# Performance work log

Measured on AMD Instinct MI355X. Metric: run time of the kernel, lower is better.

The kernel has to match this reference:

```python
import jax, jax.numpy as jnp
import numpy as np

EPS = 1e-15
MAX_NORM = 1.0 - 1e-5

def _norm(x):
    return jnp.sqrt(jnp.maximum(jnp.sum(x * x, -1, keepdims=True), EPS))

def project(x):
    n = _norm(x)
    return jnp.where(n > MAX_NORM, x * (MAX_NORM / n), x)

def mobius_add(x, y):
    x2 = jnp.sum(x * x, -1, keepdims=True)
    y2 = jnp.sum(y * y, -1, keepdims=True)
    xy = jnp.sum(x * y, -1, keepdims=True)
    num = (1.0 + 2.0 * xy + y2) * x + (1.0 - x2) * y
    den = 1.0 + 2.0 * xy + x2 * y2
    return num / jnp.maximum(den, EPS)

def expmap0(u):
    n = _norm(u)
    return jnp.tanh(n) * u / n

def expmap(u, p):
    lam = 2.0 / jnp.maximum(1.0 - jnp.sum(p * p, -1, keepdims=True), EPS)
    n = _norm(u)
    return mobius_add(p, jnp.tanh(0.5 * lam * n) * u / n)

def logmap(x, p):
    sub = mobius_add(-p, x)
    n = _norm(sub)
    lam = 2.0 / jnp.maximum(1.0 - jnp.sum(p * p, -1, keepdims=True), EPS)
    return (2.0 / lam) * jnp.arctanh(jnp.minimum(n, MAX_NORM)) * sub / n

def seg_mean(msg, idx, n):
    s = jax.ops.segment_sum(msg, idx, num_segments=n)
    c = jax.ops.segment_sum(jnp.ones((idx.shape[0], 1), msg.dtype), idx, num_segments=n)
    return s / jnp.maximum(c, 1.0)  # zero in-degree -> 0, matching DGL mean


def setup_inputs() -> dict:
    N_ENT, N_USR, N_ITM, N_REL, D = 100000, 50000, 30000, 40, 64
    E_KG, E_CF = 800000, 600000
    key = jax.random.key(0)
    ks = jax.random.split(key, 12)
    return {
        "entity_embed": 0.1 * jax.random.normal(ks[0], (N_ENT, D), jnp.float32),
        "user_embed": 0.1 * jax.random.normal(ks[1], (N_USR, D), jnp.float32),
        "relation_emb": 0.1 * jax.random.normal(ks[2], (N_REL, D), jnp.float32),
        "W1": jax.random.normal(ks[3], (D, D), jnp.float32) / np.sqrt(D),
        "W2": jax.random.normal(ks[4], (D, D), jnp.float32) / np.sqrt(D),
        "kg_src": jax.random.randint(ks[5], (E_KG,), 0, N_ENT, jnp.int32),
        "kg_dst": jax.random.randint(ks[6], (E_KG,), 0, N_ENT, jnp.int32),
        "kg_type": jax.random.randint(ks[7], (E_KG,), 0, N_REL - 2, jnp.int32),
        "iu_src": jax.random.randint(ks[8], (E_CF,), 0, N_ITM, jnp.int32),
        "iu_dst": N_ITM + jax.random.randint(ks[9], (E_CF,), 0, N_USR, jnp.int32),
        "ui_src": N_ITM + jax.random.randint(ks[10], (E_CF,), 0, N_USR, jnp.int32),
        "ui_dst": jax.random.randint(ks[11], (E_CF,), 0, N_ITM, jnp.int32),
        "n_items": N_ITM,
    }


def reference(entity_embed, user_embed, relation_emb, W1, W2,
              kg_src, kg_dst, kg_type, iu_src, iu_dst, ui_src, ui_dst, n_items):
    n_ent = entity_embed.shape[0]
    n_usr = user_embed.shape[0]
    N = n_items + n_usr

    # --- per-edge hyperbolic UDF (tan_sum) on the KG graph ---
    p = expmap0(entity_embed[kg_src])                 # [E, d] tangent origin at src
    dst_h = expmap(entity_embed[kg_dst], p)
    rel_h = expmap(relation_emb[kg_type + 2], p)
    tan_sum = logmap(project(mobius_add(dst_h, rel_h)), p)
    # sg_inv reverses edges, so mean groups by the ORIGINAL src node
    out = seg_mean(tan_sum, kg_src, n_ent)            # [n_ent, d]

    # --- CF scatter-means over item/user bipartite graphs ---
    cat_nodes = jnp.concatenate([out[:n_items], user_embed], axis=0)  # [N, d]
    u = seg_mean(cat_nodes[iu_src], iu_dst, N)[n_items:]              # [n_usr, d]

    norm_all = jnp.sum(cat_nodes * cat_nodes, -1, keepdims=True)      # ||.||^2, [N,1]
    node_n = cat_nodes / (norm_all + 1e-6)
    msg = node_n[ui_src] * norm_all[ui_dst]                           # u_mul_v
    i_cf = seg_mean(msg, ui_dst, N)[:n_items]                         # [n_items, d]

    # --- gated fusion ---
    out_items = out[:n_items]
    gi = jax.nn.sigmoid(out_items @ W1.T + i_cf @ W2.T)
    item_emb_fusion = gi * out_items + (1.0 - gi) * i_cf

    return (jnp.concatenate([item_emb_fusion, out[n_items:]], axis=0), u, out_items)
```

## Files before the change

### kernel.cpp

```cpp
#include <hip/hip_runtime.h>
#include <cstdint>

#define EPSF 1e-15f
#define MAXN (1.0f - 1e-5f)
#define BSH 9

typedef __attribute__((ext_vector_type(8))) short bf16x8;
typedef __attribute__((ext_vector_type(4))) float f32x4;
typedef unsigned short ushort_t;

__device__ __forceinline__ float wsum64(float v) {
    v += __shfl_xor(v, 1);
    v += __shfl_xor(v, 2);
    v += __shfl_xor(v, 4);
    v += __shfl_xor(v, 8);
    v += __shfl_xor(v, 16);
    v += __shfl_xor(v, 32);
    return v;
}

__device__ __forceinline__ float dot4(float4 a, float4 b) {
    return a.x * b.x + a.y * b.y + a.z * b.z + a.w * b.w;
}

__device__ __forceinline__ float frcp(float x) {
    return __builtin_amdgcn_rcpf(x);
}

__device__ __forceinline__ float tanh_f(float x) {
    x = fminf(x, 10.f);
    float t = __expf(2.f * x);
    return (t - 1.f) * frcp(t + 1.f);
}

__device__ __forceinline__ float atanh_f(float x) {
    return 0.5f * __logf((1.f + x) * frcp(1.f - x));
}

__device__ __forceinline__ ushort_t f2bf(float f) {
    uint32_t b = __float_as_uint(f);
    b = (b + 0x7FFF + ((b >> 16) & 1)) >> 16;
    return (ushort_t)b;
}

__device__ __forceinline__ float bf2f(ushort_t h) {
    return __uint_as_float((uint32_t)h << 16);
}

__device__ __forceinline__ bf16x8 pack8(const float* __restrict__ p) {
    float4 lo = *(const float4*)p;
    float4 hi = *(const float4*)(p + 4);
    bf16x8 r;
    r[0] = (short)f2bf(lo.x); r[1] = (short)f2bf(lo.y);
    r[2] = (short)f2bf(lo.z); r[3] = (short)f2bf(lo.w);
    r[4] = (short)f2bf(hi.x); r[5] = (short)f2bf(hi.y);
    r[6] = (short)f2bf(hi.z); r[7] = (short)f2bf(hi.w);
    return r;
}

__global__ __launch_bounds__(256) void cvt3_k(
        const float* __restrict__ ent, const float* __restrict__ usr,
        const float* __restrict__ rel,
        ushort_t* __restrict__ entH, ushort_t* __restrict__ usrH,
        ushort_t* __restrict__ relH, long nE, long nU, long nR) {
    long i = ((long)blockIdx.x * blockDim.x + threadIdx.x) * 8;
    const float* s; ushort_t* d; long off;
    if (i < nE) { s = ent; d = entH; off = i; }
    else if (i < nE + nU) { s = usr; d = usrH; off = i - nE; }
    else if (i < nE + nU + nR) { s = rel; d = relH; off = i - nE - nU; }
    else return;
    float4 a = *(const float4*)(s + off);
    float4 b = *(const float4*)(s + off + 4);
    ushort4 lo; lo.x = f2bf(a.x); lo.y = f2bf(a.y); lo.z = f2bf(a.z); lo.w = f2bf(a.w);
    ushort4 hi; hi.x = f2bf(b.x); hi.y = f2bf(b.y); hi.z = f2bf(b.z); hi.w = f2bf(b.w);
    *(ushort4*)(d + off) = lo;
    *(ushort4*)(d + off + 4) = hi;
}


__global__ __launch_bounds__(256) void p1_hist_k(
        const int* __restrict__ kg_src, const int* __restrict__ iu_dst,
        const int* __restrict__ ui_dst, int* __restrict__ H,
        int E_kg, int E_iu, int E_ui, int n_items, int S1, int SU, int nbins) {
    __shared__ int h[512];
    int tid = threadIdx.x;
    h[tid] = 0; h[tid + 256] = 0;
    __syncthreads();
    long tot = (long)E_kg + E_iu + E_ui;
    long b0 = (long)blockIdx.x * 2048 + tid;
#pragma unroll
    for (int j = 0; j < 8; ++j) {
        long t = b0 + (long)j * 256;
        if (t < tot) {
            int slot;
            if (t < E_kg) slot = kg_src[t];
            else if (t < (long)E_kg + E_iu) slot = S1 + iu_dst[t - E_kg] - n_items;
            else slot = S1 + SU + ui_dst[t - E_kg - E_iu];
            atomicAdd(&h[slot >> BSH], 1);
        }
    }
    __syncthreads();
    int* row = H + (size_t)blockIdx.x * nbins;
    if (tid < nbins) row[tid] = h[tid];
    if (tid + 256 < nbins) row[tid + 256] = h[tid + 256];
}

__global__ __launch_bounds__(256) void p2a_scan_k(int* __restrict__ H,
        int* __restrict__ binTotal, int NBLK, int nbins) {
    int bin = blockIdx.x, tid = threadIdx.x;
    int lane = tid & 63, w = tid >> 6;
    __shared__ int wtot[4];
    int carry = 0;
    for (int c0 = 0; c0 < NBLK; c0 += 256) {
        int idx = c0 + tid;
        int v = (idx < NBLK) ? H[(size_t)idx * nbins + bin] : 0;
        int inc = v;
#pragma unroll
        for (int off = 1; off < 64; off <<= 1) {
            int u = __shfl_up(inc, off);
            if (lane >= off) inc += u;
        }
        if (lane == 63) wtot[w] = inc;
        __syncthreads();
        int woff = 0;
        for (int i = 0; i < w; ++i) woff += wtot[i];
        int ctot = wtot[0] + wtot[1] + wtot[2] + wtot[3];
        if (idx < NBLK) H[(size_t)idx * nbins + bin] = carry + woff + inc - v;
        carry += ctot;
        __syncthreads();
    }
    if (tid == 0) binTotal[bin] = carry;
}

__global__ __launch_bounds__(512) void p2b_bins_k(const int* __restrict__ binTotal,
        int* __restrict__ binStart, int nbins) {
    int tid = threadIdx.x, lane = tid & 63, w = tid >> 6;
    __shared__ int wtot[8];
    int v = (tid < nbins) ? binTotal[tid] : 0;
    int inc = v;
#pragma unroll
    for (int off = 1; off < 64; off <<= 1) {
        int u = __shfl_up(inc, off);
        if (lane >= off) inc += u;
    }
    if (lane == 63) wtot[w] = inc;
    __syncthreads();
    int woff = 0;
    for (int i = 0; i < w; ++i) woff += wtot[i];
    if (tid < nbins) binStart[tid] = woff + inc - v;
    if (tid == 0) {
        int tot = 0;
        for (int i = 0; i < 8; ++i) tot += wtot[i];
        binStart[nbins] = tot;
    }
}

__global__ __launch_bounds__(256) void p3_scat_k(
        const int* __restrict__ kg_src, const int* __restrict__ kg_dst,
        const int* __restrict__ kg_typ, const int* __restrict__ iu_src,
        const int* __restrict__ iu_dst, const int* __restrict__ ui_src,
        const int* __restrict__ ui_dst,
        const int* __restrict__ H, const int* __restrict__ binStart,
        int2* __restrict__ recA,
        int E_kg, int E_iu, int E_ui, int n_items, int S1, int SU, int nbins) {
    __shared__ int off[512];
    int tid = threadIdx.x;
    const int* row = H + (size_t)blockIdx.x * nbins;
    if (tid < nbins) off[tid] = binStart[tid] + row[tid];
    if (tid + 256 < nbins) off[tid + 256] = binStart[tid + 256] + row[tid + 256];
    __syncthreads();
    long tot = (long)E_kg + E_iu + E_ui;
    long b0 = (long)blockIdx.x * 2048 + tid;
#pragma unroll
    for (int j = 0; j < 8; ++j) {
        long t = b0 + (long)j * 256;
        if (t < tot) {
            int slot, aux;
            if (t < E_kg) {
                slot = kg_src[t];
                aux = kg_dst[t] | ((kg_typ[t] + 2) << 18);
            } else if (t < (long)E_kg + E_iu) {
                long e = t - E_kg;
                slot = S1 + iu_dst[e] - n_items;
                aux = iu_src[e];
            } else {
                long e = t - E_kg - E_iu;
                slot = S1 + SU + ui_dst[e];
                aux = ui_src[e];
            }
            int pos = atomicAdd(&off[slot >> BSH], 1);
            recA[pos] = make_int2(slot, aux);
        }
    }
}

__global__ __launch_bounds__(256) void p4_sort_k(
        const int2* __restrict__ recA, const int* __restrict__ binStart,
        int2* __restrict__ recB, int* __restrict__ deg, int* __restrict__ base,
        int nbins) {
    int b = blockIdx.x, tid = threadIdx.x;
    int lane = tid & 63, w = tid >> 6;
    int lo = binStart[b], cnt = binStart[b + 1] - lo;
    __shared__ int h[512];
    __shared__ int pre[512];
    __shared__ int wtot[4];
    h[tid] = 0; h[tid + 256] = 0;
    __syncthreads();
    for (int i = tid; i < cnt; i += 256)
        atomicAdd(&h[recA[lo + i].x & 511], 1);
    __syncthreads();
    int v1 = h[tid];
    int inc = v1;
#pragma unroll
    for (int off = 1; off < 64; off <<= 1) {
        int u = __shfl_up(inc, off);
        if (lane >= off) inc += u;
    }
    if (lane == 63) wtot[w] = inc;
    __syncthreads();
    int woff = 0;
    for (int i = 0; i < w; ++i) woff += wtot[i];
    int T1 = wtot[0] + wtot[1] + wtot[2] + wtot[3];
    int p1 = woff + inc - v1;
    __syncthreads();
    int v2 = h[tid + 256];
    inc = v2;
#pragma unroll
    for (int off = 1; off < 64; off <<= 1) {
        int u = __shfl_up(inc, off);
        if (lane >= off) inc += u;
    }
    if (lane == 63) wtot[w] = inc;
    __syncthreads();
    woff = 0;
    for (int i = 0; i < w; ++i) woff += wtot[i];
    int p2 = T1 + woff + inc - v2;
    pre[tid] = p1; pre[tid + 256] = p2;
    int slot0 = (b << BSH) + tid;
    deg[slot0] = v1;       base[slot0] = lo + p1;
    deg[slot0 + 256] = v2; base[slot0 + 256] = lo + p2;
    __syncthreads();
    for (int i = tid; i < cnt; i += 256) {
        int2 r = recA[lo + i];
        int p = atomicAdd(&pre[r.x & 511], 1);
        recB[lo + p] = r;
    }
}


__global__ __launch_bounds__(256) void kg_edge_fused_k(const float* __restrict__ ent,
                          const float* __restrict__ rel,
                          const int2* __restrict__ rec,
                          float4* __restrict__ payload,
                          int nE) {
    int w = blockIdx.x * 4 + (threadIdx.x >> 6);
    int l = threadIdx.x & 63;
    int slot = w * 16 + (l >> 2);
    if (slot >= nE) return;
    int j0 = l & 3;
    int2 rc = rec[slot];
    int s = rc.x, d = rc.y & 0x3FFFF, ty = rc.y >> 18;
    const float4* pu = (const float4*)(ent + (size_t)s * 64);
    const float4* pv = (const float4*)(ent + (size_t)d * 64);
    const float4* pr = (const float4*)(rel + (size_t)ty * 64);

    float uu = 0.f, vv = 0.f, rr = 0.f, uv = 0.f, ur = 0.f, vr = 0.f;
#pragma unroll
    for (int i = 0; i < 4; ++i) {
        float4 a = pu[4 * i + j0], b = pv[4 * i + j0], c = pr[4 * i + j0];
        uu += dot4(a, a); vv += dot4(b, b); rr += dot4(c, c);
        uv += dot4(a, b); ur += dot4(a, c); vr += dot4(b, c);
    }
#pragma unroll
    for (int m = 1; m < 4; m <<= 1) {
        uu += __shfl_xor(uu, m);
        vv += __shfl_xor(vv, m);
        rr += __shfl_xor(rr, m);
        uv += __shfl_xor(uv, m);
        ur += __shfl_xor(ur, m);
        vr += __shfl_xor(vr, m);
    }

    float n0 = sqrtf(fmaxf(uu, EPSF));
    float cp = tanh_f(n0) * frcp(n0);
    float p2 = cp * cp * uu;
    float om_p2 = 1.f - p2;
    float lam = 2.f * frcp(fmaxf(om_p2, EPSF));

    float nv = sqrtf(fmaxf(vv, EPSF));
    float cd = tanh_f(0.5f * lam * nv) * frcp(nv);
    float wd2 = cd * cd * vv;
    float pwd = cp * cd * uv;
    float iDd = frcp(fmaxf(1.f + 2.f * pwd + p2 * wd2, EPSF));
    float a1 = (1.f + 2.f * pwd + wd2) * cp * iDd;
    float b1 = om_p2 * cd * iDd;

    float nr = sqrtf(fmaxf(rr, EPSF));
    float cr = tanh_f(0.5f * lam * nr) * frcp(nr);
    float wr2 = cr * cr * rr;
    float pwr = cp * cr * ur;
    float iDr = frcp(fmaxf(1.f + 2.f * pwr + p2 * wr2, EPSF));
    float a2 = (1.f + 2.f * pwr + wr2) * cp * iDr;
    float c2 = om_p2 * cr * iDr;

    float x2 = a1 * a1 * uu + 2.f * a1 * b1 * uv + b1 * b1 * vv;
    float y2 = a2 * a2 * uu + 2.f * a2 * c2 * ur + c2 * c2 * rr;
    float xy = a1 * a2 * uu + a1 * c2 * ur + b1 * a2 * uv + b1 * c2 * vr;
    float iden = frcp(fmaxf(1.f + 2.f * xy + x2 * y2, EPSF));
    float E = (1.f + 2.f * xy + y2) * iden;
    float F = (1.f - x2) * iden;
    float zu = E * a1 + F * a2;
    float zv = E * b1;
    float zr = F * c2;

    float z2 = zu * zu * uu + zv * zv * vv + zr * zr * rr
             + 2.f * (zu * zv * uv + zu * zr * ur + zv * zr * vr);
    float nz = sqrtf(fmaxf(z2, EPSF));
    if (nz > MAXN) {
        float sc = MAXN * frcp(nz);
        zu *= sc; zv *= sc; zr *= sc;
        z2 *= sc * sc;
    }

    float mxy = -cp * (zu * uu + zv * uv + zr * ur);
    float idenl = frcp(fmaxf(1.f + 2.f * mxy + p2 * z2, EPSF));
    float G = (1.f + 2.f * mxy + z2) * idenl;
    float H = om_p2 * idenl;
    float su = -G * cp + H * zu;
    float sv = H * zv;
    float sr = H * zr;

    float ns2 = su * su * uu + sv * sv * vv + sr * sr * rr
              + 2.f * (su * sv * uv + su * sr * ur + sv * sr * vr);
    float ns = sqrtf(fmaxf(ns2, EPSF));
    float k = fmaxf(om_p2, EPSF) * atanh_f(fminf(ns, MAXN)) * frcp(ns);

    if (j0 == 0) {
        payload[slot] = make_float4(k * sv, k * sr, k * su, __int_as_float(rc.y));
    }
}

__global__ void kg_gather_k(const float* __restrict__ ent,
                            const ushort_t* __restrict__ entH,
                            const ushort_t* __restrict__ relH,
                            const int* __restrict__ deg,
                            const int* __restrict__ base,
                            const float4* __restrict__ payload,
                            float* __restrict__ out_final,
                            float* __restrict__ out_items,
                            ushort_t* __restrict__ catH,
                            float* __restrict__ normv,
                            int n_items, int n) {
    int w = blockIdx.x * (blockDim.x >> 6) + (threadIdx.x >> 6);
    int i0 = w * 2;
    if (i0 >= n) return;
    bool has1 = (i0 + 1 < n);
    int l = threadIdx.x & 63;
    int b0 = base[i0];
    int d0 = deg[i0];
    int d1 = has1 ? deg[i0 + 1] : 0;
    int cnt = d0 + d1;
    int split = b0 + d0;
    float acc0 = 0.f, as0 = 0.f, acc1 = 0.f, as1 = 0.f;
    int q = 0;
    for (; q + 8 <= cnt; q += 8) {
        float4 p[8]; float vv[8], rr_[8];
#pragma unroll
        for (int j = 0; j < 8; ++j) p[j] = payload[b0 + q + j];
#pragma unroll
        for (int j = 0; j < 8; ++j) {
            int wd = __float_as_int(p[j].w);
            vv[j] = bf2f(entH[(size_t)(wd & 0x3FFFF) * 64 + l]);
            rr_[j] = bf2f(relH[(size_t)(wd >> 18) * 64 + l]);
        }
#pragma unroll
        for (int j = 0; j < 8; ++j) {
            float t = p[j].x * vv[j] + p[j].y * rr_[j];
            bool s0 = (b0 + q + j) < split;
            acc0 += s0 ? t : 0.f;
            acc1 += s0 ? 0.f : t;
            as0 += s0 ? p[j].z : 0.f;
            as1 += s0 ? 0.f : p[j].z;
        }
    }
    for (; q < cnt; ++q) {
        float4 p = payload[b0 + q];
        int wd = __float_as_int(p.w);
        float t = p.x * bf2f(entH[(size_t)(wd & 0x3FFFF) * 64 + l])
                + p.y * bf2f(relH[(size_t)(wd >> 18) * 64 + l]);
        bool s0 = (b0 + q) < split;
        acc0 += s0 ? t : 0.f;
        acc1 += s0 ? 0.f : t;
        as0 += s0 ? p.z : 0.f;
        as1 += s0 ? 0.f : p.z;
    }
    {
        float v = (acc0 + as0 * ent[(size_t)i0 * 64 + l]) * frcp(fmaxf((float)d0, 1.f));
        if (i0 < n_items) {
            out_items[(size_t)i0 * 64 + l] = v;
            catH[(size_t)i0 * 64 + l] = f2bf(v);
            float s2 = wsum64(v * v);
            if (l == 0) normv[i0] = s2;
        } else {
            out_final[(size_t)i0 * 64 + l] = v;
        }
    }
    if (has1) {
        int i1 = i0 + 1;
        float v = (acc1 + as1 * ent[(size_t)i1 * 64 + l]) * frcp(fmaxf((float)d1, 1.f));
        if (i1 < n_items) {
            out_items[(size_t)i1 * 64 + l] = v;
            catH[(size_t)i1 * 64 + l] = f2bf(v);
            float s2 = wsum64(v * v);
            if (l == 0) normv[i1] = s2;
        } else {
            out_final[(size_t)i1 * 64 + l] = v;
        }
    }
}

__global__ void user_norm_k(const float* __restrict__ user, float* __restrict__ normv,
                            int n_items, int n_usr) {
    int j = blockIdx.x * (blockDim.x >> 6) + (threadIdx.x >> 6);
    if (j >= n_usr) return;
    int l = threadIdx.x & 63;
    float c = user[(size_t)j * 64 + l];
    float s = wsum64(c * c);
    if (l == 0) normv[n_items + j] = s;
}


__global__ void iu_gather_k(const ushort_t* __restrict__ catH,
                            const int* __restrict__ deg, const int* __restrict__ base,
                            const int2* __restrict__ rec,
                            float* __restrict__ out_u, int n, int SOFF) {
    int w = blockIdx.x * (blockDim.x >> 6) + (threadIdx.x >> 6);
    int i0 = w * 2;
    if (i0 >= n) return;
    bool has1 = (i0 + 1 < n);
    int l = threadIdx.x & 63;
    int b0 = base[SOFF + i0];
    int d0 = deg[SOFF + i0];
    int d1 = has1 ? deg[SOFF + i0 + 1] : 0;
    int cnt = d0 + d1;
    int split = b0 + d0;
    float acc0 = 0.f, acc1 = 0.f;
    int q = 0;
    for (; q + 8 <= cnt; q += 8) {
        float vs[8]; bool s0[8];
#pragma unroll
        for (int j = 0; j < 8; ++j) {
            int sidx = rec[b0 + q + j].y;
            vs[j] = bf2f(catH[(size_t)sidx * 64 + l]);
            s0[j] = (b0 + q + j) < split;
        }
#pragma unroll
        for (int j = 0; j < 8; ++j) {
            acc0 += s0[j] ? vs[j] : 0.f;
            acc1 += s0[j] ? 0.f : vs[j];
        }
    }
    for (; q < cnt; ++q) {
        int sidx = rec[b0 + q].y;
        float v = bf2f(catH[(size_t)sidx * 64 + l]);
        bool s0 = (b0 + q) < split;
        acc0 += s0 ? v : 0.f;
        acc1 += s0 ? 0.f : v;
    }
    out_u[(size_t)i0 * 64 + l] = acc0 * frcp(fmaxf((float)d0, 1.f));
    if (has1)
        out_u[(size_t)(i0 + 1) * 64 + l] = acc1 * frcp(fmaxf((float)d1, 1.f));
}

__global__ void ui_gather_k(const ushort_t* __restrict__ catH,
                            const float* __restrict__ normv,
                            const int* __restrict__ deg, const int* __restrict__ base,
                            const int2* __restrict__ rec,
                            float* __restrict__ icf, int n, int SOFF) {
    int w = blockIdx.x * (blockDim.x >> 6) + (threadIdx.x >> 6);
    int i0 = w * 2;
    if (i0 >= n) return;
    bool has1 = (i0 + 1 < n);
    int l = threadIdx.x & 63;
    int b0 = base[SOFF + i0];
    int d0 = deg[SOFF + i0];
    int d1 = has1 ? deg[SOFF + i0 + 1] : 0;
    int cnt = d0 + d1;
    int split = b0 + d0;
    float acc0 = 0.f, acc1 = 0.f;
    int q = 0;
    for (; q + 8 <= cnt; q += 8) {
        int ss[8]; float fs[8], vs[8]; bool s0[8];
#pragma unroll
        for (int j = 0; j < 8; ++j) ss[j] = rec[b0 + q + j].y;
#pragma unroll
        for (int j = 0; j < 8; ++j) fs[j] = frcp(normv[ss[j]] + 1e-6f);
#pragma unroll
        for (int j = 0; j < 8; ++j) {
            vs[j] = bf2f(catH[(size_t)ss[j] * 64 + l]);
            s0[j] = (b0 + q + j) < split;
        }
#pragma unroll
        for (int j = 0; j < 8; ++j) {
            float t = fs[j] * vs[j];
            acc0 += s0[j] ? t : 0.f;
            acc1 += s0[j] ? 0.f : t;
        }
    }
    for (; q < cnt; ++q) {
        int sidx = rec[b0 + q].y;
        float t = frcp(normv[sidx] + 1e-6f) * bf2f(catH[(size_t)sidx * 64 + l]);
        bool s0 = (b0 + q) < split;
        acc0 += s0 ? t : 0.f;
        acc1 += s0 ? 0.f : t;
    }
    icf[(size_t)i0 * 64 + l] = normv[i0] * acc0 * frcp(fmaxf((float)d0, 1.f));
    if (has1)
        icf[(size_t)(i0 + 1) * 64 + l] =
            normv[i0 + 1] * acc1 * frcp(fmaxf((float)d1, 1.f));
}

__global__ __launch_bounds__(256) void fusion_mfma_k(const float* __restrict__ items,
                          const float* __restrict__ icf,
                          const float* __restrict__ W1, const float* __restrict__ W2,
                          float* __restrict__ outf, int n_items) {
    int lane = threadIdx.x & 63;
    int row0 = blockIdx.x * 64 + (threadIdx.x >> 6) * 16;
    int r = lane & 15, g = lane >> 4;

    int arow = row0 + r;
    size_t rbase = (size_t)(arow < n_items ? arow : 0) * 64;

    bf16x8 afrag[4];
#pragma unroll
    for (int s = 0; s < 4; ++s) {
        int kb = s * 32 + g * 8;
        const float* p = (kb < 64) ? (items + rbase + kb) : (icf + rbase + kb - 64);
        afrag[s] = pack8(p);
    }

    bf16x8 bfrag[4][4];
#pragma unroll
    for (int c = 0; c < 4; ++c) {
        int col = c * 16 + r;
#pragma unroll
        for (int s = 0; s < 4; ++s) {
            int kb = s * 32 + g * 8;
            const float* p = (kb < 64) ? (W1 + col * 64 + kb) : (W2 + col * 64 + kb - 64);
            bfrag[c][s] = pack8(p);
        }
    }

    f32x4 acc[4] = {{0.f,0.f,0.f,0.f},{0.f,0.f,0.f,0.f},
                    {0.f,0.f,0.f,0.f},{0.f,0.f,0.f,0.f}};
#pragma unroll
    for (int s = 0; s < 4; ++s)
#pragma unroll
        for (int c = 0; c < 4; ++c)
            acc[c] = __builtin_amdgcn_mfma_f32_16x16x32_bf16(afrag[s], bfrag[c][s],
                                                             acc[c], 0, 0, 0);

#pragma unroll
    for (int c = 0; c < 4; ++c) {
        int col = c * 16 + r;
#pragma unroll
        for (int q = 0; q < 4; ++q) {
            int orow = row0 + g * 4 + q;
            if (orow < n_items) {
                size_t off = (size_t)orow * 64 + col;
                float oi = items[off], cf = icf[off];
                float gate = frcp(1.f + __expf(-acc[c][q]));
                outf[off] = gate * oi + (1.f - gate) * cf;
            }
        }
    }
}

extern "C" void kernel_launch(void* const* d_in, const int* in_sizes, int n_in,
                              void* d_out, int out_size, void* d_ws, size_t ws_size,
                              hipStream_t stream) {
    const float* ent    = (const float*)d_in[0];
    const float* usr    = (const float*)d_in[1];
    const float* rel    = (const float*)d_in[2];
    const float* W1     = (const float*)d_in[3];
    const float* W2     = (const float*)d_in[4];
    const int*   kg_src = (const int*)d_in[5];
    const int*   kg_dst = (const int*)d_in[6];
    const int*   kg_typ = (const int*)d_in[7];
    const int*   iu_src = (const int*)d_in[8];
    const int*   iu_dst = (const int*)d_in[9];
    const int*   ui_src = (const int*)d_in[10];
    const int*   ui_dst = (const int*)d_in[11];

    const int n_ent   = in_sizes[0] / 64;
    const int n_usr   = in_sizes[1] / 64;
    const int n_rel   = in_sizes[2] / 64;
    const int E_kg    = in_sizes[5];
    const int E_iu    = in_sizes[8];
    const int E_ui    = in_sizes[10];
    const int n_items = (out_size - in_sizes[0] - in_sizes[1]) / 64;
    const int N       = n_items + n_usr;

    const int S1 = ((n_ent + 511) / 512) * 512;
    const int SU = ((n_usr + 511) / 512) * 512;
    const int SI = ((n_items + 511) / 512) * 512;
    const int S3 = S1 + SU + SI;
    const int nbins = S3 >> BSH;
    const long tot = (long)E_kg + E_iu + E_ui;
    const int NBLK = (int)((tot + 2047) / 2048);

    float* out_final = (float*)d_out;
    float* out_u     = out_final + (size_t)n_ent * 64;
    float* out_items = out_u + (size_t)n_usr * 64;

    int2* recA = (int2*)out_u;
    int*  H    = (int*)(recA + tot);

    float* ws = (float*)d_ws;
    size_t o = 0;
    int* binTotal = (int*)(ws + o); o += nbins;
    int* binStart = (int*)(ws + o); o += nbins + 1;
    int* deg      = (int*)(ws + o); o += S3;
    int* basep    = (int*)(ws + o); o += S3;
    o = (o + 3) & ~(size_t)3;
    int2* recB    = (int2*)(ws + o); o += (size_t)tot * 2;
    float4* pay_kg = (float4*)(ws + o); o += (size_t)E_kg * 4;
    float* icf    = (float*)pay_kg;
    float* normv  = ws + o; o += N;
    o = (o + 3) & ~(size_t)3;
    ushort_t* entH = (ushort_t*)(ws + o); o += (size_t)n_ent * 32;
    ushort_t* catH = (ushort_t*)(ws + o); o += (size_t)N * 32;
    ushort_t* relH = (ushort_t*)(ws + o); o += (size_t)n_rel * 32;
    ushort_t* usrH = catH + (size_t)n_items * 64;

    long nE64 = (long)n_ent * 64, nU64 = (long)n_usr * 64, nR64 = (long)n_rel * 64;
    long tcvt = (nE64 + nU64 + nR64) / 8;
    cvt3_k<<<(int)((tcvt + 255) / 256), 256, 0, stream>>>(ent, usr, rel,
                                                          entH, usrH, relH,
                                                          nE64, nU64, nR64);

    p1_hist_k<<<NBLK, 256, 0, stream>>>(kg_src, iu_dst, ui_dst, H,
                                        E_kg, E_iu, E_ui, n_items, S1, SU, nbins);
    p2a_scan_k<<<nbins, 256, 0, stream>>>(H, binTotal, NBLK, nbins);
    p2b_bins_k<<<1, 512, 0, stream>>>(binTotal, binStart, nbins);
    p3_scat_k<<<NBLK, 256, 0, stream>>>(kg_src, kg_dst, kg_typ, iu_src, iu_dst,
                                        ui_src, ui_dst, H, binStart, recA,
                                        E_kg, E_iu, E_ui, n_items, S1, SU, nbins);
    p4_sort_k<<<nbins, 256, 0, stream>>>(recA, binStart, recB, deg, basep, nbins);

    kg_edge_fused_k<<<(E_kg + 63) / 64, 256, 0, stream>>>(ent, rel, recB,
                                                          pay_kg, E_kg);
    int wv_e = (n_ent + 1) / 2;
    kg_gather_k<<<(wv_e + 3) / 4, 256, 0, stream>>>(ent, entH, relH, deg, basep,
                                                    pay_kg, out_final, out_items,
                                                    catH, normv, n_items, n_ent);
    user_norm_k<<<(n_usr + 3) / 4, 256, 0, stream>>>(usr, normv, n_items, n_usr);

    int wv_u = (n_usr + 1) / 2;
    iu_gather_k<<<(wv_u + 3) / 4, 256, 0, stream>>>(catH, deg, basep, recB,
                                                    out_u, n_usr, S1);
    int wv_i = (n_items + 1) / 2;
    ui_gather_k<<<(wv_i + 3) / 4, 256, 0, stream>>>(catH, normv, deg, basep, recB,
                                                    icf, n_items, S1 + SU);
    fusion_mfma_k<<<(n_items + 63) / 64, 256, 0, stream>>>(out_items, icf, W1, W2,
                                                           out_final, n_items);
}
```

Measured before the change: 238.0 us.

## Gather KG neighbors from fp32 tables and drop entity bf16 conversion

The entity and relation bf16 shadow copies are removed, so the KG gather reads the fp32 entity and relation tables directly and the conversion kernel now only converts user embeddings. The gather kernel goes back to one node per wavefront with a 4-way unrolled loop, replacing the two-nodes-per-wave split with 8-way unrolling. This saves the conversion pass over 100k×64 floats and restores fp32 precision for the KG aggregation. In exchange each gathered row costs twice the bytes (256 B instead of 128 B), and fewer independent loads are in flight per wave.

```diff
diff --git a/kernel.cpp b/kernel.cpp
--- a/kernel.cpp
+++ b/kernel.cpp
@@ -58,23 +58,16 @@
     return r;
 }
 
-__global__ __launch_bounds__(256) void cvt3_k(
-        const float* __restrict__ ent, const float* __restrict__ usr,
-        const float* __restrict__ rel,
-        ushort_t* __restrict__ entH, ushort_t* __restrict__ usrH,
-        ushort_t* __restrict__ relH, long nE, long nU, long nR) {
+__global__ __launch_bounds__(256) void cvt_usr_k(
+        const float* __restrict__ usr, ushort_t* __restrict__ usrH, long nU) {
     long i = ((long)blockIdx.x * blockDim.x + threadIdx.x) * 8;
-    const float* s; ushort_t* d; long off;
-    if (i < nE) { s = ent; d = entH; off = i; }
-    else if (i < nE + nU) { s = usr; d = usrH; off = i - nE; }
-    else if (i < nE + nU + nR) { s = rel; d = relH; off = i - nE - nU; }
-    else return;
-    float4 a = *(const float4*)(s + off);
-    float4 b = *(const float4*)(s + off + 4);
+    if (i >= nU) return;
+    float4 a = *(const float4*)(usr + i);
+    float4 b = *(const float4*)(usr + i + 4);
     ushort4 lo; lo.x = f2bf(a.x); lo.y = f2bf(a.y); lo.z = f2bf(a.z); lo.w = f2bf(a.w);
     ushort4 hi; hi.x = f2bf(b.x); hi.y = f2bf(b.y); hi.z = f2bf(b.z); hi.w = f2bf(b.w);
-    *(ushort4*)(d + off) = lo;
-    *(ushort4*)(d + off + 4) = hi;
+    *(ushort4*)(usrH + i) = lo;
+    *(ushort4*)(usrH + i + 4) = hi;
 }
 
 
@@ -341,8 +334,7 @@
 }
 
 __global__ void kg_gather_k(const float* __restrict__ ent,
-                            const ushort_t* __restrict__ entH,
-                            const ushort_t* __restrict__ relH,
+                            const float* __restrict__ rel,
                             const int* __restrict__ deg,
                             const int* __restrict__ base,
                             const float4* __restrict__ payload,
@@ -351,71 +343,46 @@
                             ushort_t* __restrict__ catH,
                             float* __restrict__ normv,
                             int n_items, int n) {
-    int w = blockIdx.x * (blockDim.x >> 6) + (threadIdx.x >> 6);
-    int i0 = w * 2;
-    if (i0 >= n) return;
-    bool has1 = (i0 + 1 < n);
+    int i = blockIdx.x * (blockDim.x >> 6) + (threadIdx.x >> 6);
+    if (i >= n) return;
     int l = threadIdx.x & 63;
-    int b0 = base[i0];
-    int d0 = deg[i0];
-    int d1 = has1 ? deg[i0 + 1] : 0;
-    int cnt = d0 + d1;
-    int split = b0 + d0;
-    float acc0 = 0.f, as0 = 0.f, acc1 = 0.f, as1 = 0.f;
+    int b = base[i], dg = deg[i];
+    float acc = 0.f, as = 0.f;
     int q = 0;
-    for (; q + 8 <= cnt; q += 8) {
-        float4 p[8]; float vv[8], rr_[8];
-#pragma unroll
-        for (int j = 0; j < 8; ++j) p[j] = payload[b0 + q + j];
-#pragma unroll
-        for (int j = 0; j < 8; ++j) {
-            int wd = __float_as_int(p[j].w);
-            vv[j] = bf2f(entH[(size_t)(wd & 0x3FFFF) * 64 + l]);
-            rr_[j] = bf2f(relH[(size_t)(wd >> 18) * 64 + l]);
-        }
-#pragma unroll
-        for (int j = 0; j < 8; ++j) {
-            float t = p[j].x * vv[j] + p[j].y * rr_[j];
-            bool s0 = (b0 + q + j) < split;
-            acc0 += s0 ? t : 0.f;
-            acc1 += s0 ? 0.f : t;
-            as0 += s0 ? p[j].z : 0.f;
-            as1 += s0 ? 0.f : p[j].z;
-        }
-    }
-    for (; q < cnt; ++q) {
-        float4 p = payload[b0 + q];
-        int wd = __float_as_int(p.w);
-        float t = p.x * bf2f(entH[(size_t)(wd & 0x3FFFF) * 64 + l])
-                + p.y * bf2f(relH[(size_t)(wd >> 18) * 64 + l]);
-        bool s0 = (b0 + q) < split;
-        acc0 += s0 ? t : 0.f;
-        acc1 += s0 ? 0.f : t;
-        as0 += s0 ? p.z : 0.f;
-        as1 += s0 ? 0.f : p.z;
-    }
-    {
-        float v = (acc0 + as0 * ent[(size_t)i0 * 64 + l]) * frcp(fmaxf((float)d0, 1.f));
-        if (i0 < n_items) {
-            out_items[(size_t)i0 * 64 + l] = v;
-            catH[(size_t)i0 * 64 + l] = f2bf(v);
-            float s2 = wsum64(v * v);
-            if (l == 0) normv[i0] = s2;
-        } else {
-            out_final[(size_t)i0 * 64 + l] = v;
-        }
-    }
-    if (has1) {
-        int i1 = i0 + 1;
-        float v = (acc1 + as1 * ent[(size_t)i1 * 64 + l]) * frcp(fmaxf((float)d1, 1.f));
-        if (i1 < n_items) {
-            out_items[(size_t)i1 * 64 + l] = v;
-            catH[(size_t)i1 * 64 + l] = f2bf(v);
-            float s2 = wsum64(v * v);
-            if (l == 0) normv[i1] = s2;
-        } else {
-            out_final[(size_t)i1 * 64 + l] = v;
-        }
+    for (; q + 4 <= dg; q += 4) {
+        float4 p0 = payload[b + q];
+        float4 p1 = payload[b + q + 1];
+        float4 p2 = payload[b + q + 2];
+        float4 p3 = payload[b + q + 3];
+        int w0 = __float_as_int(p0.w), w1 = __float_as_int(p1.w);
+        int w2 = __float_as_int(p2.w), w3 = __float_as_int(p3.w);
+        float v0 = ent[(size_t)(w0 & 0x3FFFF) * 64 + l];
+        float r0 = rel[(size_t)(w0 >> 18) * 64 + l];
+        float v1 = ent[(size_t)(w1 & 0x3FFFF) * 64 + l];
+        float r1 = rel[(size_t)(w1 >> 18) * 64 + l];
+        float v2 = ent[(size_t)(w2 & 0x3FFFF) * 64 + l];
+        float r2 = rel[(size_t)(w2 >> 18) * 64 + l];
+        float v3 = ent[(size_t)(w3 & 0x3FFFF) * 64 + l];
+        float r3 = rel[(size_t)(w3 >> 18) * 64 + l];
+        acc += p0.x * v0 + p0.y * r0 + p1.x * v1 + p1.y * r1;
+        acc += p2.x * v2 + p2.y * r2 + p3.x * v3 + p3.y * r3;
+        as += (p0.z + p1.z) + (p2.z + p3.z);
+    }
+    for (; q < dg; ++q) {
+        float4 p = payload[b + q];
+        int w = __float_as_int(p.w);
+        acc += p.x * ent[(size_t)(w & 0x3FFFF) * 64 + l]
+             + p.y * rel[(size_t)(w >> 18) * 64 + l];
+        as += p.z;
+    }
+    float v = (acc + as * ent[(size_t)i * 64 + l]) * frcp(fmaxf((float)dg, 1.f));
+    if (i < n_items) {
+        out_items[(size_t)i * 64 + l] = v;
+        catH[(size_t)i * 64 + l] = f2bf(v);
+        float s2 = wsum64(v * v);
+        if (l == 0) normv[i] = s2;
+    } else {
+        out_final[(size_t)i * 64 + l] = v;
     }
 }
 
@@ -594,7 +561,6 @@
 
     const int n_ent   = in_sizes[0] / 64;
     const int n_usr   = in_sizes[1] / 64;
-    const int n_rel   = in_sizes[2] / 64;
     const int E_kg    = in_sizes[5];
     const int E_iu    = in_sizes[8];
     const int E_ui    = in_sizes[10];
@@ -628,16 +594,11 @@
     float* icf    = (float*)pay_kg;
     float* normv  = ws + o; o += N;
     o = (o + 3) & ~(size_t)3;
-    ushort_t* entH = (ushort_t*)(ws + o); o += (size_t)n_ent * 32;
     ushort_t* catH = (ushort_t*)(ws + o); o += (size_t)N * 32;
-    ushort_t* relH = (ushort_t*)(ws + o); o += (size_t)n_rel * 32;
     ushort_t* usrH = catH + (size_t)n_items * 64;
 
-    long nE64 = (long)n_ent * 64, nU64 = (long)n_usr * 64, nR64 = (long)n_rel * 64;
-    long tcvt = (nE64 + nU64 + nR64) / 8;
-    cvt3_k<<<(int)((tcvt + 255) / 256), 256, 0, stream>>>(ent, usr, rel,
-                                                          entH, usrH, relH,
-                                                          nE64, nU64, nR64);
+    long nU64 = (long)n_usr * 64;
+    cvt_usr_k<<<(int)((nU64 / 8 + 255) / 256), 256, 0, stream>>>(usr, usrH, nU64);
 
     p1_hist_k<<<NBLK, 256, 0, stream>>>(kg_src, iu_dst, ui_dst, H,
                                         E_kg, E_iu, E_ui, n_items, S1, SU, nbins);
@@ -650,10 +611,9 @@
 
     kg_edge_fused_k<<<(E_kg + 63) / 64, 256, 0, stream>>>(ent, rel, recB,
                                                           pay_kg, E_kg);
-    int wv_e = (n_ent + 1) / 2;
-    kg_gather_k<<<(wv_e + 3) / 4, 256, 0, stream>>>(ent, entH, relH, deg, basep,
-                                                    pay_kg, out_final, out_items,
-                                                    catH, normv, n_items, n_ent);
+    kg_gather_k<<<(n_ent + 3) / 4, 256, 0, stream>>>(ent, rel, deg, basep, pay_kg,
+                                                     out_final, out_items, catH,
+                                                     normv, n_items, n_ent);
     user_norm_k<<<(n_usr + 3) / 4, 256, 0, stream>>>(usr, normv, n_items, n_usr);
 
     int wv_u = (n_usr + 1) / 2;
```

Result: faster. 230.3 us (-3.3%).
